# Kernel optimization log

Measured on AMD Instinct MI355X. Metric: run time of the kernel, lower is better.

Reference implementation:

```python
import jax, jax.numpy as jnp
import numpy as np

# Skeleton / block hyperparameters (match init_kwargs)
J = 24      # joints (chain skeleton)
CIN = 8     # in_channels_per_joint
COUT = 8    # out_channels_per_joint
K = 3       # temporal kernel size (padding = K//2, 'same')
B = 128     # batch
T = 4096    # frames
NEG_SLOPE = 0.2

# adj_list: chain neighbors including self
ADJ = [sorted({max(j - 1, 0), j, min(j + 1, J - 1)}) for j in range(J)]


def _build_masks():
    # mask[out_block_j, in_block_i] = 1 iff joint i in adj_list[j]
    m = np.zeros((J * COUT, J * CIN), np.float32)
    mo = np.zeros((J * COUT, J * 3), np.float32)
    for j in range(J):
        for i in ADJ[j]:
            m[j * COUT:(j + 1) * COUT, i * CIN:(i + 1) * CIN] = 1.0
            mo[j * COUT:(j + 1) * COUT, i * 3:(i + 1) * 3] = 1.0
    return jnp.asarray(m), jnp.asarray(mo)

MASK, MASK_OFF = _build_masks()


def setup_inputs() -> dict:
    key = jax.random.key(0)
    k0, k1, k2, k3, k4 = jax.random.split(key, 5)
    x = jax.random.normal(k0, (B, J * CIN, T), jnp.float32)      # motion features
    offset = jax.random.normal(k1, (B, J * 3), jnp.float32)      # static bone offsets
    W = jax.random.normal(k2, (J * COUT, J * CIN, K), jnp.float32) * 0.05
    b = jax.random.normal(k3, (J * COUT,), jnp.float32) * 0.01
    W_off = jax.random.normal(k4, (J * COUT, J * 3), jnp.float32) * 0.05
    return {"x": x, "offset": offset, "W": W, "b": b, "W_off": W_off}


def reference(x, offset, W, b, W_off):
    # --- SkeletalConv: adjacency-masked temporal conv1d + masked offset injection ---
    Wm = W * MASK[:, :, None]                                    # zero non-neighbor weights
    y = jax.lax.conv_general_dilated(
        x, Wm, window_strides=(1,), padding=((K // 2, K // 2),),
        dimension_numbers=("NCH", "OIH", "NCH"))                 # [B, J*COUT, T]
    off = offset @ (W_off * MASK_OFF).T                          # [B, J*COUT]
    y = y + off[:, :, None] + b[None, :, None]
    # --- SkeletalPooling: average channel blocks of merged edge regions (pairs) ---
    Bv = y.shape[0]
    y = y.reshape(Bv, J // 2, 2, COUT, T).mean(axis=2)           # pool_regions = pairs
    y = y.reshape(Bv, (J // 2) * COUT, T)                        # [B, 96, T]
    # --- LeakyReLU(0.2) ---
    return jnp.where(y > 0, y, NEG_SLOPE * y)
```

## Files before the change

kernel.cpp:

```cpp
#include <hip/hip_runtime.h>


#define NJ    24
#define NCIN  8
#define NCOUT 8
#define KS    3
#define NB    128
#define NT    4096
#define NREG  12
#define VT    8
#define TPB   256
#define TILE  (TPB * VT)
#define NTILES (NT / TILE)
#define NEG_SLOPE 0.2f

__global__ __launch_bounds__(TPB) void skel_enc_kernel(
    const float* __restrict__ x,
    const float* __restrict__ offset,
    const float* __restrict__ W,
    const float* __restrict__ bias,
    const float* __restrict__ Woff,
    float* __restrict__ out)
{
    const int tile = blockIdx.x;
    const int r    = blockIdx.y;
    const int b    = blockIdx.z;

    const int jlo  = (2 * r - 1 > 0) ? (2 * r - 1) : 0;
    const int jhi  = (2 * r + 2 < NJ - 1) ? (2 * r + 2) : (NJ - 1);
    const int ncin = (jhi - jlo + 1) * NCIN;
    const int c0   = jlo * NCIN;

    __shared__ __align__(16) float sW[32 * 24];
    __shared__ float sBias[NCOUT];

    const int tid = threadIdx.x;
    const int j0 = 2 * r, j1 = 2 * r + 1;

    for (int idx = tid; idx < 32 * 24; idx += TPB) {
        const int c   = idx / 24;
        const int rem = idx - c * 24;
        const int o   = rem / 3;
        const int k   = rem - o * 3;
        float val = 0.f;
        if (c < ncin) {
            const int gj = jlo + (c >> 3);
            const int gc = c0 + c;
            const float w0 = W[(size_t)(j0 * NCOUT + o) * (NJ * NCIN * KS) + gc * KS + k];
            const float w1 = W[(size_t)(j1 * NCOUT + o) * (NJ * NCIN * KS) + gc * KS + k];
            const float m0 = (gj >= j0 - 1 && gj <= j0 + 1) ? 1.f : 0.f;
            const float m1 = (gj >= j1 - 1 && gj <= j1 + 1) ? 1.f : 0.f;
            val = 0.5f * (w0 * m0 + w1 * m1);
        }
        sW[idx] = val;
    }

    if (tid < NCOUT) {
        const int o = tid;
        float acc = 0.5f * (bias[j0 * NCOUT + o] + bias[j1 * NCOUT + o]);
        const float* offb = offset + (size_t)b * (NJ * 3);
        float s0 = 0.f, s1 = 0.f;
        for (int i = 0; i < NJ * 3; ++i) {
            const int ji = i / 3;
            const float ov = offb[i];
            if (ji >= j0 - 1 && ji <= j0 + 1)
                s0 += Woff[(size_t)(j0 * NCOUT + o) * (NJ * 3) + i] * ov;
            if (ji >= j1 - 1 && ji <= j1 + 1)
                s1 += Woff[(size_t)(j1 * NCOUT + o) * (NJ * 3) + i] * ov;
        }
        sBias[o] = acc + 0.5f * (s0 + s1);
    }
    __syncthreads();

    const int t0 = tile * TILE + tid * VT;

    float acc[NCOUT][VT];
    #pragma unroll
    for (int o = 0; o < NCOUT; ++o) {
        const float bv = sBias[o];
        #pragma unroll
        for (int v = 0; v < VT; ++v) acc[o][v] = bv;
    }

    const float* xb = x + (size_t)b * (NJ * NCIN) * NT + t0;
    const bool has_lo = (t0 > 0);
    const bool has_hi = (t0 + VT < NT);

    for (int c = 0; c < ncin; ++c) {
        const float* xp = xb + (size_t)(c0 + c) * NT;

        float xv[VT + 2];
        const float4 a0 = *reinterpret_cast<const float4*>(xp);
        const float4 a1 = *reinterpret_cast<const float4*>(xp + 4);
        xv[1] = a0.x; xv[2] = a0.y; xv[3] = a0.z; xv[4] = a0.w;
        xv[5] = a1.x; xv[6] = a1.y; xv[7] = a1.z; xv[8] = a1.w;
        {
            const float xm = xp[has_lo ? -1 : 0];
            xv[0] = has_lo ? xm : 0.f;
            const float xq = xp[has_hi ? VT : VT - 1];
            xv[VT + 1] = has_hi ? xq : 0.f;
        }

        float wreg[24];
        {
            float4* wr = reinterpret_cast<float4*>(wreg);
            const float4* sw = reinterpret_cast<const float4*>(&sW[c * 24]);
            #pragma unroll
            for (int q = 0; q < 6; ++q) wr[q] = sw[q];
        }

        #pragma unroll
        for (int o = 0; o < NCOUT; ++o) {
            #pragma unroll
            for (int k = 0; k < KS; ++k) {
                const float wv = wreg[o * 3 + k];
                #pragma unroll
                for (int v = 0; v < VT; ++v)
                    acc[o][v] = fmaf(wv, xv[v + k], acc[o][v]);
            }
        }
    }

    float* ob = out + ((size_t)b * (NREG * NCOUT) + r * NCOUT) * NT + t0;
    #pragma unroll
    for (int o = 0; o < NCOUT; ++o) {
        float4 s0, s1;
        float tmp[VT];
        #pragma unroll
        for (int v = 0; v < VT; ++v) {
            const float y = acc[o][v];
            tmp[v] = (y > 0.f) ? y : NEG_SLOPE * y;
        }
        s0.x = tmp[0]; s0.y = tmp[1]; s0.z = tmp[2]; s0.w = tmp[3];
        s1.x = tmp[4]; s1.y = tmp[5]; s1.z = tmp[6]; s1.w = tmp[7];
        float* op = ob + (size_t)o * NT;
        *reinterpret_cast<float4*>(op)     = s0;
        *reinterpret_cast<float4*>(op + 4) = s1;
    }
}

extern "C" void kernel_launch(void* const* d_in, const int* in_sizes, int n_in,
                              void* d_out, int out_size, void* d_ws, size_t ws_size,
                              hipStream_t stream) {
    const float* x      = (const float*)d_in[0];
    const float* offset = (const float*)d_in[1];
    const float* W      = (const float*)d_in[2];
    const float* bias   = (const float*)d_in[3];
    const float* Woff   = (const float*)d_in[4];
    float* out = (float*)d_out;

    dim3 grid(NTILES, NREG, NB);
    skel_enc_kernel<<<grid, TPB, 0, stream>>>(x, offset, W, bias, Woff, out);
}
```

Baseline: 653.2 us.

## Split output channels across two thread halves and fix channel loop to 32

Each block now covers half as many time steps, and its two 128-thread halves each compute 4 of the 8 pooled output channels. This halves per-thread accumulator registers and doubles the number of blocks. The channel loop is fixed at 32 iterations with clamped indices and zero-padded weights, so edge regions run extra work with zero weights. Weights are read from shared memory each iteration instead of being staged into registers, and both thread halves load the same x data, which doubles x traffic through the cache.

```diff
diff --git a/kernel.cpp b/kernel.cpp
--- a/kernel.cpp
+++ b/kernel.cpp
@@ -9,9 +9,11 @@
 #define NT    4096
 #define NREG  12
 #define VT    8
+#define LANES 128
 #define TPB   256
-#define TILE  (TPB * VT)
+#define TILE  (LANES * VT)
 #define NTILES (NT / TILE)
+#define NCH   32
 #define NEG_SLOPE 0.2f
 
 __global__ __launch_bounds__(TPB) void skel_enc_kernel(
@@ -25,115 +27,113 @@
     const int tile = blockIdx.x;
     const int r    = blockIdx.y;
     const int b    = blockIdx.z;
+    const int tid  = threadIdx.x;
 
-    const int jlo  = (2 * r - 1 > 0) ? (2 * r - 1) : 0;
-    const int jhi  = (2 * r + 2 < NJ - 1) ? (2 * r + 2) : (NJ - 1);
+    const int j0 = 2 * r, j1 = 2 * r + 1;
+    const int jlo  = (j0 - 1 > 0) ? (j0 - 1) : 0;
+    const int jhi  = (j1 + 1 < NJ - 1) ? (j1 + 1) : (NJ - 1);
     const int ncin = (jhi - jlo + 1) * NCIN;
     const int c0   = jlo * NCIN;
 
-    __shared__ __align__(16) float sW[32 * 24];
+    __shared__ float sW[NCH * 24];
     __shared__ float sBias[NCOUT];
 
-    const int tid = threadIdx.x;
-    const int j0 = 2 * r, j1 = 2 * r + 1;
+    for (int idx = tid; idx < NCH * 24; idx += TPB) sW[idx] = 0.f;
+    __syncthreads();
 
-    for (int idx = tid; idx < 32 * 24; idx += TPB) {
-        const int c   = idx / 24;
-        const int rem = idx - c * 24;
-        const int o   = rem / 3;
-        const int k   = rem - o * 3;
-        float val = 0.f;
-        if (c < ncin) {
-            const int gj = jlo + (c >> 3);
-            const int gc = c0 + c;
-            const float w0 = W[(size_t)(j0 * NCOUT + o) * (NJ * NCIN * KS) + gc * KS + k];
-            const float w1 = W[(size_t)(j1 * NCOUT + o) * (NJ * NCIN * KS) + gc * KS + k];
-            const float m0 = (gj >= j0 - 1 && gj <= j0 + 1) ? 1.f : 0.f;
-            const float m1 = (gj >= j1 - 1 && gj <= j1 + 1) ? 1.f : 0.f;
-            val = 0.5f * (w0 * m0 + w1 * m1);
+    for (int jj = 0; jj < 2; ++jj) {
+        const int j = j0 + jj;
+        for (int idx = tid; idx < NCOUT * 96; idx += TPB) {
+            const int o   = idx / 96;
+            const int pos = idx - o * 96;
+            const int c   = pos / 3;
+            const int k   = pos - 3 * c;
+            const int gj  = jlo + (c >> 3);
+            float val = 0.f;
+            if (c < ncin && gj >= j - 1 && gj <= j + 1)
+                val = 0.5f * W[(size_t)(j * NCOUT + o) * (192 * 3) + (size_t)(c0 + c) * 3 + k];
+            sW[c * 24 + o * 3 + k] += val;
         }
-        sW[idx] = val;
+        __syncthreads();
     }
 
     if (tid < NCOUT) {
         const int o = tid;
-        float acc = 0.5f * (bias[j0 * NCOUT + o] + bias[j1 * NCOUT + o]);
+        float acc0 = 0.5f * (bias[j0 * NCOUT + o] + bias[j1 * NCOUT + o]);
         const float* offb = offset + (size_t)b * (NJ * 3);
-        float s0 = 0.f, s1 = 0.f;
-        for (int i = 0; i < NJ * 3; ++i) {
+        const int ilo = ((j0 - 1 > 0) ? (j0 - 1) : 0) * 3;
+        const int jtop = (j1 + 1 < NJ - 1) ? (j1 + 1) : (NJ - 1);
+        const int ihi = (jtop + 1) * 3;
+        float s = 0.f;
+        for (int i = ilo; i < ihi; ++i) {
             const int ji = i / 3;
             const float ov = offb[i];
-            if (ji >= j0 - 1 && ji <= j0 + 1)
-                s0 += Woff[(size_t)(j0 * NCOUT + o) * (NJ * 3) + i] * ov;
-            if (ji >= j1 - 1 && ji <= j1 + 1)
-                s1 += Woff[(size_t)(j1 * NCOUT + o) * (NJ * 3) + i] * ov;
+            float w = 0.f;
+            if (ji >= j0 - 1 && ji <= j0 + 1) w += Woff[(size_t)(j0 * NCOUT + o) * (NJ * 3) + i];
+            if (ji >= j1 - 1 && ji <= j1 + 1) w += Woff[(size_t)(j1 * NCOUT + o) * (NJ * 3) + i];
+            s += w * ov;
         }
-        sBias[o] = acc + 0.5f * (s0 + s1);
+        sBias[o] = acc0 + 0.5f * s;
     }
     __syncthreads();
 
-    const int t0 = tile * TILE + tid * VT;
+    const int lane = tid & (LANES - 1);
+    const int ob   = (tid >> 7) * 4;
+    const int t0   = tile * TILE + lane * VT;
 
-    float acc[NCOUT][VT];
+    float acc[4][VT];
     #pragma unroll
-    for (int o = 0; o < NCOUT; ++o) {
-        const float bv = sBias[o];
+    for (int ol = 0; ol < 4; ++ol) {
+        const float bv = sBias[ob + ol];
         #pragma unroll
-        for (int v = 0; v < VT; ++v) acc[o][v] = bv;
+        for (int v = 0; v < VT; ++v) acc[ol][v] = bv;
     }
 
     const float* xb = x + (size_t)b * (NJ * NCIN) * NT + t0;
     const bool has_lo = (t0 > 0);
     const bool has_hi = (t0 + VT < NT);
 
-    for (int c = 0; c < ncin; ++c) {
-        const float* xp = xb + (size_t)(c0 + c) * NT;
+    #pragma unroll 1
+    for (int c = 0; c < NCH; ++c) {
+        const int gc = (c0 + c < 191) ? (c0 + c) : 191;
+        const float* xp = xb + (size_t)gc * NT;
 
         float xv[VT + 2];
         const float4 a0 = *reinterpret_cast<const float4*>(xp);
         const float4 a1 = *reinterpret_cast<const float4*>(xp + 4);
         xv[1] = a0.x; xv[2] = a0.y; xv[3] = a0.z; xv[4] = a0.w;
         xv[5] = a1.x; xv[6] = a1.y; xv[7] = a1.z; xv[8] = a1.w;
-        {
-            const float xm = xp[has_lo ? -1 : 0];
-            xv[0] = has_lo ? xm : 0.f;
-            const float xq = xp[has_hi ? VT : VT - 1];
-            xv[VT + 1] = has_hi ? xq : 0.f;
-        }
+        const float xm = xp[has_lo ? -1 : 0];
+        xv[0] = has_lo ? xm : 0.f;
+        const float xq = xp[has_hi ? VT : VT - 1];
+        xv[VT + 1] = has_hi ? xq : 0.f;
 
-        float wreg[24];
-        {
-            float4* wr = reinterpret_cast<float4*>(wreg);
-            const float4* sw = reinterpret_cast<const float4*>(&sW[c * 24]);
-            #pragma unroll
-            for (int q = 0; q < 6; ++q) wr[q] = sw[q];
-        }
-
+        const int wbase = c * 24 + ob * 3;
         #pragma unroll
-        for (int o = 0; o < NCOUT; ++o) {
+        for (int ol = 0; ol < 4; ++ol) {
             #pragma unroll
             for (int k = 0; k < KS; ++k) {
-                const float wv = wreg[o * 3 + k];
+                const float wv = sW[wbase + ol * 3 + k];
                 #pragma unroll
                 for (int v = 0; v < VT; ++v)
-                    acc[o][v] = fmaf(wv, xv[v + k], acc[o][v]);
+                    acc[ol][v] = fmaf(wv, xv[v + k], acc[ol][v]);
             }
         }
     }
 
-    float* ob = out + ((size_t)b * (NREG * NCOUT) + r * NCOUT) * NT + t0;
+    float* obase = out + ((size_t)b * (NREG * NCOUT) + (size_t)(r * NCOUT + ob)) * NT + t0;
     #pragma unroll
-    for (int o = 0; o < NCOUT; ++o) {
+    for (int ol = 0; ol < 4; ++ol) {
         float4 s0, s1;
-        float tmp[VT];
-        #pragma unroll
-        for (int v = 0; v < VT; ++v) {
-            const float y = acc[o][v];
-            tmp[v] = (y > 0.f) ? y : NEG_SLOPE * y;
-        }
-        s0.x = tmp[0]; s0.y = tmp[1]; s0.z = tmp[2]; s0.w = tmp[3];
-        s1.x = tmp[4]; s1.y = tmp[5]; s1.z = tmp[6]; s1.w = tmp[7];
-        float* op = ob + (size_t)o * NT;
+        s0.x = acc[ol][0] > 0.f ? acc[ol][0] : NEG_SLOPE * acc[ol][0];
+        s0.y = acc[ol][1] > 0.f ? acc[ol][1] : NEG_SLOPE * acc[ol][1];
+        s0.z = acc[ol][2] > 0.f ? acc[ol][2] : NEG_SLOPE * acc[ol][2];
+        s0.w = acc[ol][3] > 0.f ? acc[ol][3] : NEG_SLOPE * acc[ol][3];
+        s1.x = acc[ol][4] > 0.f ? acc[ol][4] : NEG_SLOPE * acc[ol][4];
+        s1.y = acc[ol][5] > 0.f ? acc[ol][5] : NEG_SLOPE * acc[ol][5];
+        s1.z = acc[ol][6] > 0.f ? acc[ol][6] : NEG_SLOPE * acc[ol][6];
+        s1.w = acc[ol][7] > 0.f ? acc[ol][7] : NEG_SLOPE * acc[ol][7];
+        float* op = obase + (size_t)ol * NT;
         *reinterpret_cast<float4*>(op)     = s0;
         *reinterpret_cast<float4*>(op + 4) = s1;
     }
```

New measurement: 738.6 us. 13.1% more time.
